# Kernel tuning notes

Measured on AMD Instinct MI355X. Metric: run time of the kernel, lower is better.

## Reference

```python
import jax, jax.numpy as jnp
import numpy as np
from math import factorial

N_SCALES = 4
N_ORI = 4
NA = 9            # spatial_corr_width
H_IMG = 1024
P_REAL = max(2 * N_ORI, 5)


def _polar_grid(H, W):
    ctr_y = int(np.ceil((H + 0.5) / 2)); ctr_x = int(np.ceil((W + 0.5) / 2))
    y = (np.arange(1, H + 1) - ctr_y) / (H / 2.0)
    x = (np.arange(1, W + 1) - ctr_x) / (W / 2.0)
    xr, yr = np.meshgrid(x, y)
    angle = np.arctan2(yr, xr)
    rad = np.sqrt(xr ** 2 + yr ** 2)
    rad[ctr_y - 1, ctr_x - 1] = rad[ctr_y - 1, ctr_x - 2]  # avoid log2(0)
    return np.log2(rad), angle


def _hi(log_rad, shift):
    # raised-cosine sqrt highpass mask: transition over log_rad in [shift-1, shift]
    return np.cos(np.pi / 2.0 * np.clip(log_rad - shift, -1.0, 0.0))


def _lo(log_rad, shift):
    h = _hi(log_rad, shift)
    return np.sqrt(np.clip(1.0 - h * h, 0.0, 1.0))


def _crop(dims):
    # pyrtools-style frequency-domain downsample-by-2 crop indices
    dims = np.asarray(dims)
    ctr = np.ceil((dims + 0.5) / 2).astype(int)
    lodims = np.ceil((dims - 0.5) / 2).astype(int)
    loctr = np.ceil((lodims + 0.5) / 2).astype(int)
    s = ctr - loctr
    return s[0], s[0] + lodims[0], s[1], s[1] + lodims[1]


def _build_pyramid(im):
    """Complex steerable pyramid (frequency-domain), non tight-frame."""
    order = N_ORI - 1
    const = (2.0 ** (2 * order)) * factorial(order) ** 2 / (N_ORI * factorial(2 * order))
    lr, ang = _polar_grid(*im.shape)
    imdft = jnp.fft.fftshift(jnp.fft.fft2(im))
    hipass = jnp.fft.ifft2(jnp.fft.ifftshift(imdft * jnp.asarray(_hi(lr, 0.0), jnp.float32))).real
    lodft = imdft * jnp.asarray(_lo(lr, 0.0), jnp.float32)
    bands, recon_dfts = [], []
    for s in range(N_SCALES):
        recon_dfts.append(lodft)  # spectrum of scales >= s content (partial recon)
        shift = -(s + 1)
        hm = _hi(lr, shift)
        sb = []
        for b in range(N_ORI):
            a = np.mod(ang - np.pi * b / N_ORI + np.pi, 2 * np.pi) - np.pi
            am = 2.0 * np.sqrt(const) * (np.cos(a) ** order) * (np.abs(a) < np.pi / 2)
            banddft = ((-1j) ** order) * lodft * jnp.asarray(hm * am, jnp.float32)
            sb.append(jnp.fft.ifft2(jnp.fft.ifftshift(banddft)))
        bands.append(sb)
        y0, y1, x0, x1 = _crop(lodft.shape)
        lr, ang = lr[y0:y1, x0:x1], ang[y0:y1, x0:x1]
        lodft = lodft[y0:y1, x0:x1] * jnp.asarray(_lo(lr, shift), jnp.float32)
    lowpass = jnp.fft.ifft2(jnp.fft.ifftshift(lodft)).real
    recons = [jnp.fft.ifft2(jnp.fft.ifftshift(d)).real for d in recon_dfts] + [lowpass]
    return hipass, bands, lowpass, recons


def _autocorr(x):
    # central NA x NA window of the autocorrelation, via FFT
    x = x - x.mean()
    H, W = x.shape
    F = jnp.fft.fft2(x)
    p = F.real ** 2 + F.imag ** 2
    ac = jnp.fft.fftshift(jnp.fft.ifft2(p).real) / (H * W)
    lz = NA // 2
    return jax.lax.dynamic_slice(ac, (H // 2 - lz, W // 2 - lz), (NA, NA))


def _skew_kurt(x):
    mu = x.mean()
    c = x - mu
    v = (c * c).mean()
    return (c ** 3).mean() / v ** 1.5, (c ** 4).mean() / v ** 2, v


def _norm_cc(A, B):
    # true cross-correlation of centered columns
    C = A.T @ B / A.shape[0]
    sa = jnp.sqrt((A * A).mean(0)); sb = jnp.sqrt((B * B).mean(0))
    return C / (sa[:, None] * sb[None, :] + 1e-12)


def _expand2(x):
    H, W = x.shape
    F = jnp.fft.fftshift(jnp.fft.fft2(x))
    pad = jnp.zeros((2 * H, 2 * W), F.dtype).at[H // 2:H // 2 + H, W // 2:W // 2 + W].set(F)
    return jnp.fft.ifft2(jnp.fft.ifftshift(pad)) * 4.0


def _ps_stats(image):
    im = image[0, 0]
    hipass, bands, lowpass, recons = _build_pyramid(im)
    sk, ku, var = _skew_kurt(im)
    pix = jnp.stack([im.mean(), var, sk, ku, im.min(), im.max()])
    mags = [[jnp.abs(bands[s][b]) for b in range(N_ORI)] for s in range(N_SCALES)]
    mag_means = jnp.stack([jnp.abs(hipass).mean()]
                          + [mags[s][b].mean() for s in range(N_SCALES) for b in range(N_ORI)]
                          + [jnp.abs(lowpass).mean()])
    mags = [[m - m.mean() for m in row] for row in mags]
    lz = NA // 2
    acm = jnp.zeros((NA, NA, N_SCALES, N_ORI), jnp.float32)
    for s in range(N_SCALES):
        for b in range(N_ORI):
            ac = _autocorr(mags[s][b])
            acm = acm.at[:, :, s, b].set(ac / (ac[lz, lz] + 1e-12))
    acr = jnp.zeros((NA, NA, N_SCALES + 1), jnp.float32)
    skew_r, kurt_r, std_r = [], [], []
    for s, r in enumerate(recons):
        ac = _autocorr(r)
        acr = acr.at[:, :, s].set(ac / (ac[lz, lz] + 1e-12))
        sk_, ku_, v_ = _skew_kurt(r)
        skew_r.append(sk_); kurt_r.append(ku_); std_r.append(jnp.sqrt(v_))
    com = jnp.zeros((N_ORI, N_ORI, N_SCALES + 1), jnp.float32)
    csm = jnp.zeros((N_ORI, N_ORI, N_SCALES), jnp.float32)
    cor = jnp.zeros((P_REAL, P_REAL, N_SCALES + 1), jnp.float32)
    csr = jnp.zeros((2 * N_ORI, P_REAL, N_SCALES), jnp.float32)
    for s in range(N_SCALES):
        M = jnp.stack([m.ravel() for m in mags[s]], 1)                      # (N, Nor) centered magnitudes
        R = jnp.stack([(bands[s][b].real - bands[s][b].real.mean()).ravel()
                       for b in range(N_ORI)], 1)                            # (N, Nor) real parts
        com = com.at[:, :, s].set(_norm_cc(M, M))
        cor = cor.at[:N_ORI, :N_ORI, s].set(_norm_cc(R, R))
        if s < N_SCALES - 1:
            ups = [_expand2(bands[s + 1][b]) for b in range(N_ORI)]
            dp = [u * u / (jnp.abs(u) + 1e-12) for u in ups]                # phase-doubled parents
            Pm = jnp.stack([(jnp.abs(u) - jnp.abs(u).mean()).ravel() for u in ups], 1)
            csm = csm.at[:, :, s].set(_norm_cc(M, Pm))
            RP = jnp.stack([d.real.ravel() for d in dp] + [d.imag.ravel() for d in dp], 1)
            RP = RP - RP.mean(0)
            csr = csr.at[:N_ORI, :2 * N_ORI, s].set(_norm_cc(R, RP))
        else:
            lp = _expand2(lowpass).real
            lp = lp - lp.mean()
            shifts = [lp, jnp.roll(lp, 2, 1), jnp.roll(lp, -2, 1), jnp.roll(lp, 2, 0), jnp.roll(lp, -2, 0)]
            RP = jnp.stack([t.ravel() for t in shifts], 1)                  # 5 shifted lowpass parents
            csr = csr.at[:N_ORI, :5, s].set(_norm_cc(R, RP))
            cor = cor.at[:5, :5, N_SCALES].set(_norm_cc(RP, RP))
    hc = hipass - hipass.mean()
    var_hp = (hc * hc).mean()
    vec = jnp.concatenate([pix, mag_means, acm.ravel(),
                           jnp.stack(skew_r), jnp.stack(kurt_r), acr.ravel(),
                           jnp.stack(std_r), com.ravel(), csm.ravel(),
                           cor.ravel(), csr.ravel(), var_hp[None]])
    return vec[None, None, :].astype(jnp.float32)  # (B=1, C=1, S=2461)


def setup_inputs():
    key = jax.random.key(0)
    return {"image": jax.random.normal(key, (1, 1, H_IMG, H_IMG), jnp.float32)}


def reference(image):
    return _ps_stats(image)
```

## Files before the change

### kernel.cpp

```cpp
#include <hip/hip_runtime.h>
#include <hip/hip_fp16.h>
#include <math.h>

#define PI_F 3.14159265358979323846f

enum { LOP_NONE=0, LOP_R2C, LOP_PAD };
enum { SOP_REAL=0, SOP_HL };

__host__ __device__ constexpr int P4(int a, int b){ return a*4 - a*(a-1)/2 + (b-a); }
__host__ __device__ constexpr int P5(int a, int b){ return a*5 - a*(a-1)/2 + (b-a); }

__device__ __forceinline__ unsigned encf(float f){
  unsigned u = __float_as_uint(f);
  return (u & 0x80000000u) ? ~u : (u | 0x80000000u);
}
__device__ __forceinline__ float decf(unsigned u){
  unsigned b = (u & 0x80000000u) ? (u ^ 0x80000000u) : ~u;
  return __uint_as_float(b);
}
__device__ __forceinline__ float2 cxmul(float2 a, float c, float s){
  return make_float2(c*a.x - s*a.y, c*a.y + s*a.x);
}
__device__ __forceinline__ float2 f2add(float2 a, float2 b){ return make_float2(a.x+b.x, a.y+b.y); }
__device__ __forceinline__ float2 f2sub(float2 a, float2 b){ return make_float2(a.x-b.x, a.y-b.y); }
__device__ __forceinline__ float2 h2f(__half2 h){ return __half22float2(h); }
__device__ __forceinline__ __half2 f2h(float2 f){ return __float22half2_rn(f); }

template<int CNT, int WAVES>
__device__ __forceinline__ void block_reduce_add(float (&acc)[CNT], double* out){
  __shared__ float red[WAVES*CNT];
  int lane = threadIdx.x & 63;
  int wid  = threadIdx.x >> 6;
  #pragma unroll
  for (int k = 0; k < CNT; k++){
    float v = acc[k];
    #pragma unroll
    for (int o = 32; o > 0; o >>= 1) v += __shfl_down(v, o, 64);
    if (lane == 0) red[wid*CNT + k] = v;
  }
  __syncthreads();
  int t = threadIdx.x;
  if (t < CNT){
    double s = 0.0;
    #pragma unroll
    for (int w = 0; w < WAVES; w++) s += (double)red[w*CNT + t];
    atomicAdd(&out[t], s);
  }
  __syncthreads();
}

template<int CNT, int WAVES>
__device__ __forceinline__ void block_reduce_add_sc(float (&acc)[CNT], double* out, float* red){
  __syncthreads();
  int lane = threadIdx.x & 63;
  int wid  = threadIdx.x >> 6;
  #pragma unroll
  for (int k = 0; k < CNT; k++){
    float v = acc[k];
    #pragma unroll
    for (int o = 32; o > 0; o >>= 1) v += __shfl_down(v, o, 64);
    if (lane == 0) red[wid*CNT + k] = v;
  }
  __syncthreads();
  int t = threadIdx.x;
  if (t < CNT){
    double s = 0.0;
    #pragma unroll
    for (int w = 0; w < WAVES; w++) s += (double)red[w*CNT + t];
    atomicAdd(&out[t], s);
  }
}

__device__ __forceinline__ void polar_f(int iy, int ix, float& lr, float& ang){
  float yn = (float)(iy - 512) * (1.f/512.f);
  float xn = (float)(ix - 512) * (1.f/512.f);
  ang = atan2f(yn, xn);
  float rad = (iy == 512 && ix == 512) ? (1.f/512.f) : sqrtf(xn*xn + yn*yn);
  lr = log2f(rad);
}
__device__ __forceinline__ float f_hi(float lr, float shift){
  float v = fminf(fmaxf(lr - shift, -1.f), 0.f);
  return cosf((PI_F*0.5f) * v);
}
__device__ __forceinline__ float f_lo(float lr, float shift){
  float h = f_hi(lr, shift);
  float q = fminf(fmaxf(1.f - h*h, 0.f), 1.f);
  return sqrtf(q);
}
__device__ __forceinline__ float band_am(float ang, int b){
  float a0 = ang - (PI_F*0.25f)*(float)b + PI_F;
  float a = fmodf(a0, 2.f*PI_F);
  if (a < 0.f) a += 2.f*PI_F;
  a -= PI_F;
  float mk = 0.f;
  if (fabsf(a) < PI_F*0.5f){ float c = cosf(a); mk = 1.78885438199983f*c*c*c; }
  return mk;
}

__device__ __forceinline__ void bfly4(float2* v, bool fwd){
  float2 A = f2add(v[0], v[2]), B = f2sub(v[0], v[2]);
  float2 C = f2add(v[1], v[3]), D = f2sub(v[1], v[3]);
  float2 dj = fwd ? make_float2(D.y, -D.x) : make_float2(-D.y, D.x);
  v[0] = f2add(A, C);
  v[1] = f2add(B, dj);
  v[2] = f2sub(A, C);
  v[3] = f2sub(B, dj);
}

template<int N, int T>
__device__ __forceinline__ void fft_rows_body(float2* sm, int t, float dir){
  const bool fwd = (dir < 0.f);
  int Ns = 1;
  if constexpr ((N & 0xAAAAAAAAu) != 0){
    constexpr int NB2 = N/2;
    constexpr int P2 = (NB2 + T - 1)/T;
    float2 a[P2], b[P2];
    #pragma unroll
    for (int p = 0; p < P2; p++){
      int q = t + p*T;
      if (q < NB2){ a[p] = sm[q]; b[p] = sm[q + N/2]; }
    }
    __syncthreads();
    #pragma unroll
    for (int p = 0; p < P2; p++){
      int q = t + p*T;
      if (q < NB2){
        sm[2*q]   = f2add(a[p], b[p]);
        sm[2*q+1] = f2sub(a[p], b[p]);
      }
    }
    __syncthreads();
    Ns = 2;
  }
  constexpr int NB4 = N/4;
  for (; Ns < N; Ns <<= 2){
    float2 v[4];
    int q = t, k = 0;
    if (q < NB4){
      k = q & (Ns - 1);
      #pragma unroll
      for (int r = 0; r < 4; r++) v[r] = sm[q + r*NB4];
      if (k){
        float ang = dir * (PI_F*0.5f) * (float)k / (float)Ns;
        float s1, c1; __sincosf(ang, &s1, &c1);
        float c2 = c1*c1 - s1*s1, s2 = 2.f*c1*s1;
        float c3 = c1*c2 - s1*s2, s3 = c1*s2 + s1*c2;
        v[1] = cxmul(v[1], c1, s1);
        v[2] = cxmul(v[2], c2, s2);
        v[3] = cxmul(v[3], c3, s3);
      }
      bfly4(v, fwd);
    }
    __syncthreads();
    if (q < NB4){
      int dd = ((q - k) << 2) + k;
      sm[dd]        = v[0];
      sm[dd + Ns]   = v[1];
      sm[dd + 2*Ns] = v[2];
      sm[dd + 3*Ns] = v[3];
    }
    __syncthreads();
  }
}

template<int N, int CB, int T>
__device__ __forceinline__ void fft_cols_body(float2* sm, int t, float dir){
  constexpr int LCB = (CB==2)?1:(CB==4)?2:(CB==8)?3:4;
  const bool fwd = (dir < 0.f);
  int Ns = 1;
  if constexpr ((N & 0xAAAAAAAAu) != 0){
    constexpr int NB2 = (N/2)*CB;
    constexpr int P2 = (NB2 + T - 1)/T;
    float2 a[P2], b[P2];
    #pragma unroll
    for (int p = 0; p < P2; p++){
      int q = t + p*T;
      if (q < NB2){
        int c = q & (CB-1), tt = q >> LCB;
        a[p] = sm[tt*CB + c];
        b[p] = sm[(tt + N/2)*CB + c];
      }
    }
    __syncthreads();
    #pragma unroll
    for (int p = 0; p < P2; p++){
      int q = t + p*T;
      if (q < NB2){
        int c = q & (CB-1), tt = q >> LCB;
        sm[(2*tt)*CB + c]   = f2add(a[p], b[p]);
        sm[(2*tt+1)*CB + c] = f2sub(a[p], b[p]);
      }
    }
    __syncthreads();
    Ns = 2;
  }
  constexpr int NB4 = (N/4)*CB;
  constexpr int PB = (NB4 + T - 1)/T;
  for (; Ns < N; Ns <<= 2){
    float2 v[PB][4];
    int kk[PB];
    #pragma unroll
    for (int p = 0; p < PB; p++){
      int q = t + p*T;
      if (q < NB4){
        int c = q & (CB-1), tt = q >> LCB;
        int k = tt & (Ns - 1);
        kk[p] = k;
        #pragma unroll
        for (int r = 0; r < 4; r++) v[p][r] = sm[(tt + r*(N/4))*CB + c];
        if (k){
          float ang = dir * (PI_F*0.5f) * (float)k / (float)Ns;
          float s1, c1; __sincosf(ang, &s1, &c1);
          float c2 = c1*c1 - s1*s1, s2 = 2.f*c1*s1;
          float c3 = c1*c2 - s1*s2, s3 = c1*s2 + s1*c2;
          v[p][1] = cxmul(v[p][1], c1, s1);
          v[p][2] = cxmul(v[p][2], c2, s2);
          v[p][3] = cxmul(v[p][3], c3, s3);
        }
        bfly4(v[p], fwd);
      }
    }
    __syncthreads();
    #pragma unroll
    for (int p = 0; p < PB; p++){
      int q = t + p*T;
      if (q < NB4){
        int c = q & (CB-1), tt = q >> LCB;
        int k = kk[p];
        int dd = ((tt - k) << 2) + k;
        sm[(dd)*CB + c]        = v[p][0];
        sm[(dd + Ns)*CB + c]   = v[p][1];
        sm[(dd + 2*Ns)*CB + c] = v[p][2];
        sm[(dd + 3*Ns)*CB + c] = v[p][3];
      }
    }
    __syncthreads();
  }
}

template<int N>
__global__ __launch_bounds__((N/4 < 64) ? 64 : N/4)
void ps_fft_rows(float2* __restrict__ dst, const void* __restrict__ vsrc,
                 int srcH1, float dir, int xin, int xout, int lop)
{
  constexpr int T = (N/4 < 64) ? 64 : N/4;
  __shared__ float2 sm[N];
  const int t = threadIdx.x;
  const int l = blockIdx.x;
  float2* dline = dst + (size_t)l*N;
  if (lop == LOP_PAD){
    const int q = N/4;
    const int sl = l - q;
    if (sl < 0 || sl >= srcH1){
      for (int j = t; j < N; j += T) dline[j] = make_float2(0.f, 0.f);
      return;
    }
    const float2* s = (const float2*)vsrc + (size_t)sl*srcH1;
    for (int j = t; j < N; j += T){
      int p = j ^ xin;
      sm[j] = (p >= q && p < q + srcH1) ? s[p - q] : make_float2(0.f, 0.f);
    }
  } else if (lop == LOP_R2C){
    const float* s = (const float*)vsrc + (size_t)l*N;
    for (int j = t; j < N; j += T) sm[j] = make_float2(s[j ^ xin], 0.f);
  } else {
    const float2* s = (const float2*)vsrc + (size_t)l*N;
    for (int j = t; j < N; j += T) sm[j] = s[j ^ xin];
  }
  __syncthreads();
  fft_rows_body<N, T>(sm, t, dir);
  for (int j = t; j < N; j += T) dline[j ^ xout] = sm[j];
}

template<int N>
__global__ __launch_bounds__((N/4 < 64) ? 64 : N/4)
void ps_fft_rows_m(__half2* __restrict__ h4, __half2* __restrict__ bandD,
                   const float2* __restrict__ lodS, const float2* __restrict__ lodS1,
                   int nA, int inAHalf, int n, int srcH1,
                   int moffB, float shiftB, int moffC, float shiftC, float scale)
{
  constexpr int T = (N/4 < 64) ? 64 : N/4;
  constexpr int XIN = N/2;
  __shared__ float2 sm[N];
  const int t = threadIdx.x;
  const int l = blockIdx.x & (N-1);
  const int img = blockIdx.x / N;
  __half2* dline;
  if (img < nA)          dline = h4 + (size_t)img*n + (size_t)l*N;
  else if (img < nA + 4) dline = bandD + (size_t)(img - nA)*n + (size_t)l*N;
  else                   dline = h4 + (size_t)(img - 4)*n + (size_t)l*N;

  if (img < nA){
    if (inAHalf){
      const __half2* s = h4 + (size_t)img*n + (size_t)l*N;
      for (int j = t; j < N; j += T) sm[j] = h2f(s[j ^ XIN]);
    } else {
      const float2* s = lodS + (size_t)l*N;
      for (int j = t; j < N; j += T) sm[j] = s[j ^ XIN];
    }
  } else if (img < nA + 4){
    const int b = img - nA;
    const float2* s = lodS + (size_t)l*N;
    for (int j = t; j < N; j += T){
      int x = j ^ XIN;
      float lr, ang; polar_f(moffB + l, moffB + x, lr, ang);
      float mf = f_hi(lr, shiftB) * band_am(ang, b);
      float2 v = s[x];
      sm[j] = make_float2(-mf*v.y, mf*v.x);
    }
  } else {
    const int b = img - nA - 4;
    const int q = N/4;
    const int sl = l - q;
    if (sl < 0 || sl >= srcH1){
      __half2 z = f2h(make_float2(0.f, 0.f));
      for (int j = t; j < N; j += T) dline[j] = z;
      return;
    }
    const float2* s = lodS1 + (size_t)sl*srcH1;
    for (int j = t; j < N; j += T){
      int p = j ^ XIN;
      float2 r = make_float2(0.f, 0.f);
      if (p >= q && p < q + srcH1){
        int x = p - q;
        float lr, ang; polar_f(moffC + sl, moffC + x, lr, ang);
        float mf = f_hi(lr, shiftC) * band_am(ang, b);
        float2 v = s[x];
        r = make_float2(-mf*v.y, mf*v.x);
      }
      sm[j] = r;
    }
  }
  __syncthreads();
  fft_rows_body<N, T>(sm, t, +1.f);
  for (int j = t; j < N; j += T){
    float2 v = sm[j];
    dline[j] = f2h(make_float2(v.x*scale, v.y*scale));
  }
}

template<int N, int CB>
__global__ __launch_bounds__(512)
void ps_fft_cols(float2* __restrict__ dst, const float2* __restrict__ src,
                 __half2* __restrict__ hdst, int hstride,
                 float dir, int xin, int xout, float scale,
                 int sop, float* __restrict__ rdst, double* __restrict__ mout)
{
  constexpr int T = 512;
  constexpr int LCB = (CB==2)?1:(CB==4)?2:(CB==8)?3:4;
  constexpr int NE = N*CB;
  __shared__ float2 sm[NE];
  const int t = threadIdx.x;
  const int c0 = blockIdx.x * CB;
  const float2* sbase = src + c0;

  for (int e = t; e < NE; e += T){
    int j = e >> LCB, c = e & (CB - 1);
    sm[e] = sbase[(size_t)(j ^ xin)*N + c];
  }
  __syncthreads();
  fft_cols_body<N, CB, T>(sm, t, dir);

  if (sop == SOP_HL){
    for (int e = t; e < NE; e += T){
      int j = e >> LCB, c = e & (CB - 1);
      int row = j ^ xout, col = c0 + c;
      float lr, ang; polar_f(row, col, lr, ang);
      float lo = f_lo(lr, 0.f), hi = f_hi(lr, 0.f);
      float2 v = sm[j*CB + c];
      float2 lv = make_float2(v.x*lo, v.y*lo);
      size_t o = (size_t)row*N + col;
      dst[o] = lv;
      hdst[o] = f2h(make_float2(v.x*hi, v.y*hi));
      hdst[(size_t)hstride + o] = f2h(lv);
    }
    return;
  }
  for (int e = t; e < NE; e += T){
    int j = e >> LCB, c = e & (CB - 1);
    rdst[(size_t)(j ^ xout)*N + c0 + c] = sm[j*CB + c].x * scale;
  }
  if (mout){
    float acc[5] = {0.f,0.f,0.f,0.f,0.f};
    for (int e = t; e < NE; e += T){
      float r = sm[e].x * scale, r2 = r*r;
      acc[0] += r; acc[1] += r2; acc[2] += r2*r; acc[3] += r2*r2; acc[4] += fabsf(r);
    }
    block_reduce_add_sc<5, 8>(acc, mout, (float*)sm);
  }
}

template<int N, int CB>
__global__ __launch_bounds__(512)
void ps_fft_cols_m(__half2* __restrict__ h4, __half2* __restrict__ bandD,
                   int nA, int n,
                   float* __restrict__ rdst, int rimg, int rmask,
                   double* __restrict__ mout, int mstride)
{
  constexpr int T = 512;
  constexpr int LCB = (CB==2)?1:(CB==4)?2:(CB==8)?3:4;
  constexpr int NBK = N / CB;
  constexpr int NE = N*CB;
  constexpr int XIN = N/2;
  __shared__ float2 sm[NE];
  const int t = threadIdx.x;
  const int img = blockIdx.x / NBK;
  const int c0 = (blockIdx.x % NBK) * CB;
  __half2* hbase;
  if (img < nA)          hbase = h4 + (size_t)img*n + c0;
  else if (img < nA + 4) hbase = bandD + (size_t)(img - nA)*n + c0;
  else                   hbase = h4 + (size_t)(img - 4)*n + c0;

  for (int e = t; e < NE; e += T){
    int j = e >> LCB, c = e & (CB - 1);
    sm[e] = h2f(hbase[(size_t)(j ^ XIN)*N + c]);
  }
  __syncthreads();
  fft_cols_body<N, CB, T>(sm, t, +1.f);

  if (img < nA){
    if ((rmask >> img) & 1){
      for (int e = t; e < NE; e += T){
        int j = e >> LCB, c = e & (CB - 1);
        rdst[(size_t)img*(size_t)rimg + (size_t)j*N + c0 + c] = sm[j*CB + c].x;
      }
    }
    float acc[5] = {0.f,0.f,0.f,0.f,0.f};
    for (int e = t; e < NE; e += T){
      float r = sm[e].x, r2 = r*r;
      acc[0] += r; acc[1] += r2; acc[2] += r2*r; acc[3] += r2*r2; acc[4] += fabsf(r);
    }
    block_reduce_add_sc<5, 8>(acc, mout + (size_t)img*mstride, (float*)sm);
  } else {
    float mul = (img < nA + 4) ? 1.f : 4.f;
    for (int e = t; e < NE; e += T){
      int j = e >> LCB, c = e & (CB - 1);
      float2 v = sm[j*CB + c];
      hbase[(size_t)j*N + c] = f2h(make_float2(v.x*mul, v.y*mul));
    }
  }
}

#define MAX_AC_TASKS 9
struct AcTaskTab {
  const void* src[MAX_AC_TASKS];
  int isMag[MAX_AC_TASKS];
  int H[MAX_AC_TASKS];
  int npi[MAX_AC_TASKS];
  int nb[MAX_AC_TASKS];
  int stOff[MAX_AC_TASKS];
  int stStride[MAX_AC_TASKS];
  int blkStart[MAX_AC_TASKS+1];
  int nTasks;
};

__global__ __launch_bounds__(256, 1)
void ps_spat_ac_multi(AcTaskTab tt, double* __restrict__ ST)
{
  __shared__ float tile[40*40];
  const int gb = blockIdx.x;
  int tk = 0;
  while (tk + 1 < tt.nTasks && gb >= tt.blkStart[tk+1]) tk++;
  const int lb  = gb - tt.blkStart[tk];
  const int nb  = tt.nb[tk];
  const int img = lb / nb;
  const int b0  = lb - img*nb;
  const int H = tt.H[tk];
  const int n_per_img = tt.npi[tk];
  const int isMag = tt.isMag[tk];
  const void* vsrc = tt.src[tk];
  const int t = threadIdx.x;
  const int tilesX = H >> 5;
  const int tiles = tilesX * tilesX;
  float acc[41];
  #pragma unroll
  for (int k = 0; k < 41; k++) acc[k] = 0.f;

  for (int tl = b0; tl < tiles; tl += nb){
    int by = tl / tilesX, bx = tl - by*tilesX;
    int y0 = by << 5, x0 = bx << 5;
    __syncthreads();
    for (int e = t; e < 40*40; e += 256){
      int ly = e / 40, lx = e - ly*40;
      int gy = (y0 + ly - 4) & (H - 1);
      int gx = (x0 + lx - 4) & (H - 1);
      float v;
      if (isMag){
        float2 c = h2f(((const __half2*)vsrc)[(size_t)img*n_per_img + (size_t)gy*H + gx]);
        v = sqrtf(c.x*c.x + c.y*c.y);
      } else {
        v = ((const float*)vsrc)[(size_t)img*n_per_img + (size_t)gy*H + gx];
      }
      tile[e] = v;
    }
    __syncthreads();
    for (int p = t; p < 32*32; p += 256){
      int py = p >> 5, px = p & 31;
      const float* row0 = tile + (py+4)*40 + (px+4);
      float c = row0[0];
      #pragma unroll
      for (int dx = 0; dx <= 4; dx++)
        acc[dx] += c * row0[dx];
      #pragma unroll
      for (int dy = 1; dy <= 4; dy++){
        const float* rw = row0 + dy*40;
        #pragma unroll
        for (int dx = -4; dx <= 4; dx++)
          acc[5 + (dy-1)*9 + (dx+4)] += c * rw[dx];
      }
    }
  }
  block_reduce_add<41, 4>(acc, ST + tt.stOff[tk] + (size_t)img*tt.stStride[tk]);
}

__global__ __launch_bounds__(256)
void ps_crop_lo(float2* dst, const float2* src, int Hs, int offNew, float shift){
  int Hd = Hs/2;
  int i = blockIdx.x*blockDim.x + threadIdx.x;
  if (i >= Hd*Hd) return;
  int y = i / Hd, x = i - y*Hd;
  float lr, ang; polar_f(offNew + y, offNew + x, lr, ang);
  float mk = f_lo(lr, shift);
  float2 v = src[(y + Hs/4)*Hs + (x + Hs/4)];
  dst[i] = make_float2(v.x*mk, v.y*mk);
}

__global__ void ps_init_mm(unsigned* mm){ mm[0] = 0xFFFFFFFFu; mm[1] = 0u; }

__global__ __launch_bounds__(256, 1)
void ps_im_stats(const float4* __restrict__ x4, int n4, double* out, unsigned* mm){
  float acc[4] = {0.f,0.f,0.f,0.f};
  float mn = INFINITY, mx = -INFINITY;
  for (int i = blockIdx.x*blockDim.x + threadIdx.x; i < n4; i += gridDim.x*blockDim.x){
    float4 v = x4[i];
    float a0 = v.x, a1 = v.y, a2 = v.z, a3 = v.w;
    acc[0] += a0 + a1 + a2 + a3;
    acc[1] += a0*a0 + a1*a1 + a2*a2 + a3*a3;
    acc[2] += a0*a0*a0 + a1*a1*a1 + a2*a2*a2 + a3*a3*a3;
    acc[3] += a0*a0*a0*a0 + a1*a1*a1*a1 + a2*a2*a2*a2 + a3*a3*a3*a3;
    mn = fminf(mn, fminf(fminf(a0,a1), fminf(a2,a3)));
    mx = fmaxf(mx, fmaxf(fmaxf(a0,a1), fmaxf(a2,a3)));
  }
  block_reduce_add<4, 4>(acc, out);
  #pragma unroll
  for (int o = 32; o > 0; o >>= 1){
    mn = fminf(mn, __shfl_down(mn, o, 64));
    mx = fmaxf(mx, __shfl_down(mx, o, 64));
  }
  if ((threadIdx.x & 63) == 0){
    atomicMin(&mm[0], encf(mn));
    atomicMax(&mm[1], encf(mx));
  }
}

struct ScaleATab { const __half2* b[4]; int n[4]; };
__global__ __launch_bounds__(256, 1)
void ps_scaleA_multi(ScaleATab tt, double* __restrict__ ST){
  int s = blockIdx.y;
  int n = tt.n[s];
  if ((size_t)blockIdx.x*blockDim.x >= (size_t)n) return;
  const __half2* bb = tt.b[s];
  double* outp = ST + 64 + s*32;
  float acc[28];
  #pragma unroll
  for (int k = 0; k < 28; k++) acc[k] = 0.f;
  for (int i = blockIdx.x*blockDim.x + threadIdx.x; i < n; i += gridDim.x*blockDim.x){
    float2 v0 = h2f(bb[i]), v1 = h2f(bb[(size_t)n + i]),
           v2 = h2f(bb[2*(size_t)n + i]), v3 = h2f(bb[3*(size_t)n + i]);
    float ab[4] = { sqrtf(v0.x*v0.x+v0.y*v0.y), sqrtf(v1.x*v1.x+v1.y*v1.y),
                    sqrtf(v2.x*v2.x+v2.y*v2.y), sqrtf(v3.x*v3.x+v3.y*v3.y) };
    float re[4] = { v0.x, v1.x, v2.x, v3.x };
    #pragma unroll
    for (int a = 0; a < 4; a++){
      #pragma unroll
      for (int c = a; c < 4; c++){
        acc[P4(a,c)]      += ab[a]*ab[c];
        acc[10 + P4(a,c)] += re[a]*re[c];
      }
      acc[20 + a] += ab[a];
      acc[24 + a] += re[a];
    }
  }
  block_reduce_add<28, 4>(acc, outp);
}
__global__ __launch_bounds__(256, 1)
void ps_scaleB(const __half2* __restrict__ u0, const __half2* __restrict__ u1,
               const __half2* __restrict__ u2, const __half2* __restrict__ u3,
               const __half2* __restrict__ s0, const __half2* __restrict__ s1,
               const __half2* __restrict__ s2, const __half2* __restrict__ s3,
               int n, double* out){
  float acc[72];
  #pragma unroll
  for (int k = 0; k < 72; k++) acc[k] = 0.f;
  for (int i = blockIdx.x*blockDim.x + threadIdx.x; i < n; i += gridDim.x*blockDim.x){
    float2 u[4] = { h2f(u0[i]), h2f(u1[i]), h2f(u2[i]), h2f(u3[i]) };
    float2 bb[4] = { h2f(s0[i]), h2f(s1[i]), h2f(s2[i]), h2f(s3[i]) };
    float au[4], dre[4], dim[4], M[4], R[4];
    #pragma unroll
    for (int c = 0; c < 4; c++){
      float xx = u[c].x, yy = u[c].y;
      float mag = sqrtf(xx*xx + yy*yy);
      float den = mag + 1e-12f;
      au[c] = mag;
      dre[c] = (xx*xx - yy*yy)/den;
      dim[c] = (2.f*xx*yy)/den;
      M[c] = sqrtf(bb[c].x*bb[c].x + bb[c].y*bb[c].y);
      R[c] = bb[c].x;
    }
    #pragma unroll
    for (int c = 0; c < 4; c++){
      acc[c]      += au[c];
      acc[4 + c]  += au[c]*au[c];
      acc[24 + c] += dre[c];
      acc[28 + c] += dim[c];
      acc[32 + c] += dre[c]*dre[c];
      acc[36 + c] += dim[c]*dim[c];
    }
    #pragma unroll
    for (int a = 0; a < 4; a++)
      #pragma unroll
      for (int c = 0; c < 4; c++){
        acc[8 + a*4 + c]  += M[a]*au[c];
        acc[40 + a*4 + c] += R[a]*dre[c];
        acc[56 + a*4 + c] += R[a]*dim[c];
      }
  }
  block_reduce_add<72, 4>(acc, out);
}
__global__ __launch_bounds__(256, 1)
void ps_scaleC(const __half2* __restrict__ s0, const __half2* __restrict__ s1,
               const __half2* __restrict__ s2, const __half2* __restrict__ s3,
               const float* __restrict__ lp, int n, double* out){
  float acc[36];
  #pragma unroll
  for (int k = 0; k < 36; k++) acc[k] = 0.f;
  for (int i = blockIdx.x*blockDim.x + threadIdx.x; i < n; i += gridDim.x*blockDim.x){
    int y = i >> 7, x = i & 127;
    float L[5];
    L[0] = lp[i];
    L[1] = lp[(y << 7) | ((x + 126) & 127)];
    L[2] = lp[(y << 7) | ((x + 2) & 127)];
    L[3] = lp[(((y + 126) & 127) << 7) | x];
    L[4] = lp[(((y + 2) & 127) << 7) | x];
    float R[4] = { h2f(s0[i]).x, h2f(s1[i]).x, h2f(s2[i]).x, h2f(s3[i]).x };
    acc[0] += L[0];
    #pragma unroll
    for (int a = 0; a < 5; a++)
      #pragma unroll
      for (int c = a; c < 5; c++)
        acc[1 + P5(a,c)] += L[a]*L[c];
    #pragma unroll
    for (int a = 0; a < 4; a++)
      #pragma unroll
      for (int j = 0; j < 5; j++)
        acc[16 + a*5 + j] += R[a]*L[j];
  }
  block_reduce_add<36, 4>(acc, out);
}

__device__ __forceinline__ double d_ns(int s){ double h = (double)(1024 >> s); return h*h; }
__device__ __forceinline__ void d_moments(const double* Mo, double n,
                                          double& sk, double& ku, double& var){
  double m = Mo[0]/n, e2 = Mo[1]/n, e3 = Mo[2]/n, e4 = Mo[3]/n;
  var = e2 - m*m;
  double c3 = e3 - 3.0*m*e2 + 2.0*m*m*m;
  double c4 = e4 - 4.0*m*e3 + 6.0*m*m*e2 - 3.0*m*m*m*m;
  sk = c3/pow(var,1.5); ku = c4/(var*var);
}
__device__ __forceinline__ int ac_o(int w){
  int dy = w/9 - 4, dx = w - (w/9)*9 - 4;
  int ady = dy, adx = dx;
  if (dy < 0 || (dy == 0 && dx < 0)){ ady = -dy; adx = -dx; }
  return (ady == 0) ? adx : (5 + (ady-1)*9 + (adx+4));
}

__global__ __launch_bounds__(256)
void ps_finalize(const double* __restrict__ ST, const unsigned* __restrict__ MM,
                 float* __restrict__ out, int out_size){
  int idx = blockIdx.x*blockDim.x + threadIdx.x;
  if (idx >= out_size) return;
  const double n0 = 1048576.0;
  double val = 0.0;

  if (idx <= 5){
    if (idx == 4){ out[4] = decf(MM[0]); return; }
    if (idx == 5){ out[5] = decf(MM[1]); return; }
    double sk, ku, v; d_moments(ST, n0, sk, ku, v);
    val = (idx == 0) ? ST[0]/n0 : (idx == 1) ? v : (idx == 2) ? sk : ku;
  } else if (idx == 6){
    val = ST[8]/n0;
  } else if (idx <= 22){
    int i = idx - 7; int s = i >> 2, b = i & 3;
    val = ST[64 + s*32 + 20 + b] / d_ns(s);
  } else if (idx == 23){
    val = ST[10 + 4*6 + 4] / 4096.0;
  } else if (idx <= 1319){
    int i = idx - 24; int w = i >> 4; int j = i & 15;
    int s = j >> 2, b = j & 3;
    double n = d_ns(s);
    const double* R = ST + 752 + j*48;
    double mu = ST[64 + s*32 + 20 + b]/n, mu2 = mu*mu;
    int o = ac_o(w);
    val = (R[o]/n - mu2) / (R[0]/n - mu2 + 1e-12);
  } else if (idx <= 1329){
    int i = idx - 1320; bool kq = (i >= 5); int r = kq ? i - 5 : i;
    double n = (r == 4) ? 4096.0 : d_ns(r);
    double sk, ku, v; d_moments(ST + 10 + r*6, n, sk, ku, v);
    val = kq ? ku : sk;
  } else if (idx <= 1734){
    int i = idx - 1330; int w = i / 5; int r = i - w*5;
    double n = (r == 4) ? 4096.0 : d_ns(r);
    const double* R = ST + 512 + r*48;
    double mu = ST[10 + r*6]/n, mu2 = mu*mu;
    int o = ac_o(w);
    val = (R[o]/n - mu2) / (R[0]/n - mu2 + 1e-12);
  } else if (idx <= 1739){
    int r = idx - 1735;
    double n = (r == 4) ? 4096.0 : d_ns(r);
    double sk, ku, v; d_moments(ST + 10 + r*6, n, sk, ku, v);
    val = sqrt(v);
  } else if (idx <= 1819){
    int i = idx - 1740; int s = i % 5; int q = i / 5; int a = q >> 2, b = q & 3;
    if (s < 4){
      double n = d_ns(s); const double* A = ST + 64 + s*32;
      double ma = A[20+a]/n, mb = A[20+b]/n;
      double caa = A[P4(a,a)]/n - ma*ma, cbb = A[P4(b,b)]/n - mb*mb;
      int lo = a < b ? a : b, hi = a < b ? b : a;
      double cab = A[P4(lo,hi)]/n - ma*mb;
      val = cab / (sqrt(caa)*sqrt(cbb) + 1e-12);
    }
  } else if (idx <= 1883){
    int i = idx - 1820; int s = i & 3; int q = i >> 2; int a = q >> 2, c = q & 3;
    if (s < 3){
      double n = d_ns(s); const double* A = ST + 64 + s*32; const double* B = ST + 192 + s*80;
      double mM = A[20+a]/n; double sdM = sqrt(A[P4(a,a)]/n - mM*mM);
      double mU = B[c]/n;    double sdU = sqrt(B[4+c]/n - mU*mU);
      val = (B[8 + a*4 + c]/n - mM*mU) / (sdM*sdU + 1e-12);
    }
  } else if (idx <= 2203){
    int i = idx - 1884; int s = i % 5; int q = i / 5; int a = q >> 3, b = q & 7;
    if (s < 4){
      if (a < 4 && b < 4){
        double n = d_ns(s); const double* A = ST + 64 + s*32;
        double ma = A[24+a]/n, mb = A[24+b]/n;
        double caa = A[10+P4(a,a)]/n - ma*ma, cbb = A[10+P4(b,b)]/n - mb*mb;
        int lo = a < b ? a : b, hi = a < b ? b : a;
        double cab = A[10+P4(lo,hi)]/n - ma*mb;
        val = cab / (sqrt(caa)*sqrt(cbb) + 1e-12);
      }
    } else {
      if (a < 5 && b < 5){
        const double* C = ST + 432; const double n3 = 16384.0;
        double lb = C[0]/n3;
        double caa = C[1+P5(a,a)]/n3 - lb*lb, cbb = C[1+P5(b,b)]/n3 - lb*lb;
        int lo = a < b ? a : b, hi = a < b ? b : a;
        double cab = C[1+P5(lo,hi)]/n3 - lb*lb;
        val = cab / (sqrt(caa)*sqrt(cbb) + 1e-12);
      }
    }
  } else if (idx <= 2459){
    int i = idx - 2204; int s = i & 3; int q = i >> 2; int a = q >> 3, c = q & 7;
    if (a < 4){
      double n = d_ns(s); const double* A = ST + 64 + s*32;
      double mR = A[24+a]/n; double sdR = sqrt(A[10+P4(a,a)]/n - mR*mR);
      if (s < 3 && c < 8){
        const double* B = ST + 192 + s*80;
        if (c < 4){
          double md = B[24+c]/n; double sd = sqrt(B[32+c]/n - md*md);
          val = (B[40 + a*4 + c]/n - mR*md) / (sdR*sd + 1e-12);
        } else {
          int cc = c - 4;
          double md = B[28+cc]/n; double sd = sqrt(B[36+cc]/n - md*md);
          val = (B[56 + a*4 + cc]/n - mR*md) / (sdR*sd + 1e-12);
        }
      } else if (s == 3 && c < 5){
        const double* C = ST + 432; const double n3 = 16384.0;
        double lb = C[0]/n3;
        double sdL = sqrt(C[1+P5(c,c)]/n3 - lb*lb);
        val = (C[16 + a*5 + c]/n3 - mR*lb) / (sdR*sdL + 1e-12);
      }
    }
  } else {
    val = ST[5]/n0 - (ST[4]/n0)*(ST[4]/n0);
  }
  out[idx] = (float)val;
}

static void rows_s(int H, float2* dst, const void* src, int srcH1,
                   float dir, int xin, int xout, int lop, hipStream_t st){
  dim3 g(H);
  switch (H){
    case 64:   ps_fft_rows<64>  <<<g, 64,  0, st>>>(dst, src, srcH1, dir, xin, xout, lop); break;
    case 128:  ps_fft_rows<128> <<<g, 64,  0, st>>>(dst, src, srcH1, dir, xin, xout, lop); break;
    case 256:  ps_fft_rows<256> <<<g, 64,  0, st>>>(dst, src, srcH1, dir, xin, xout, lop); break;
    case 512:  ps_fft_rows<512> <<<g, 128, 0, st>>>(dst, src, srcH1, dir, xin, xout, lop); break;
    case 1024: ps_fft_rows<1024><<<g, 256, 0, st>>>(dst, src, srcH1, dir, xin, xout, lop); break;
    default: break;
  }
}
static void cols_s(int H, float2* dst, const float2* src, __half2* hdst, int hstride,
                   float dir, int xin, int xout, float scale,
                   int sop, float* rdst, double* mout, hipStream_t st){
  switch (H){
    case 64:   ps_fft_cols<64,16>  <<<dim3(64/16),  512, 0, st>>>(dst, src, hdst, hstride, dir, xin, xout, scale, sop, rdst, mout); break;
    case 128:  ps_fft_cols<128,16> <<<dim3(128/16), 512, 0, st>>>(dst, src, hdst, hstride, dir, xin, xout, scale, sop, rdst, mout); break;
    case 256:  ps_fft_cols<256,16> <<<dim3(256/16), 512, 0, st>>>(dst, src, hdst, hstride, dir, xin, xout, scale, sop, rdst, mout); break;
    case 512:  ps_fft_cols<512,16> <<<dim3(512/16), 512, 0, st>>>(dst, src, hdst, hstride, dir, xin, xout, scale, sop, rdst, mout); break;
    case 1024: ps_fft_cols<1024,8> <<<dim3(1024/8), 512, 0, st>>>(dst, src, hdst, hstride, dir, xin, xout, scale, sop, rdst, mout); break;
    default: break;
  }
}
static void rows_m(int H, __half2* h4, __half2* bandD, const float2* lodS, const float2* lodS1,
                   int nA, int inAHalf, int nimg, int n, int srcH1,
                   int moffB, float shiftB, int moffC, float shiftC, float scale, hipStream_t st){
  dim3 g(nimg * H);
  switch (H){
    case 128:  ps_fft_rows_m<128> <<<g, 64,  0, st>>>(h4, bandD, lodS, lodS1, nA, inAHalf, n, srcH1, moffB, shiftB, moffC, shiftC, scale); break;
    case 256:  ps_fft_rows_m<256> <<<g, 64,  0, st>>>(h4, bandD, lodS, lodS1, nA, inAHalf, n, srcH1, moffB, shiftB, moffC, shiftC, scale); break;
    case 512:  ps_fft_rows_m<512> <<<g, 128, 0, st>>>(h4, bandD, lodS, lodS1, nA, inAHalf, n, srcH1, moffB, shiftB, moffC, shiftC, scale); break;
    case 1024: ps_fft_rows_m<1024><<<g, 256, 0, st>>>(h4, bandD, lodS, lodS1, nA, inAHalf, n, srcH1, moffB, shiftB, moffC, shiftC, scale); break;
    default: break;
  }
}
static void cols_m(int H, __half2* h4, __half2* bandD, int nA, int nimg, int n,
                   float* rdst, int rimg, int rmask, double* mout, int mstride, hipStream_t st){
  switch (H){
    case 128:  ps_fft_cols_m<128,16> <<<dim3(nimg*(128/16)), 512, 0, st>>>(h4, bandD, nA, n, rdst, rimg, rmask, mout, mstride); break;
    case 256:  ps_fft_cols_m<256,16> <<<dim3(nimg*(256/16)), 512, 0, st>>>(h4, bandD, nA, n, rdst, rimg, rmask, mout, mstride); break;
    case 512:  ps_fft_cols_m<512,16> <<<dim3(nimg*(512/16)), 512, 0, st>>>(h4, bandD, nA, n, rdst, rimg, rmask, mout, mstride); break;
    case 1024: ps_fft_cols_m<1024,8> <<<dim3(nimg*(1024/8)), 512, 0, st>>>(h4, bandD, nA, n, rdst, rimg, rmask, mout, mstride); break;
    default: break;
  }
}

static inline dim3 gr(int n){ return dim3((n + 255)/256); }
static inline int  rblocks(int n){ int b = (n + 255)/256; return b > 512 ? 512 : b; }

#define FWD (-1.0f)
#define INV (+1.0f)

extern "C" void kernel_launch(void* const* d_in, const int* in_sizes, int n_in,
                              void* d_out, int out_size, void* d_ws, size_t ws_size,
                              hipStream_t stream){
  (void)in_sizes; (void)n_in;
  const float* im = (const float*)d_in[0];
  float* out = (float*)d_out;

  const int Hs[5]   = {1024, 512, 256, 128, 64};
  const int offs[5] = {0, 256, 384, 448, 480};

  char* base = (char*)d_ws;
  size_t off = 0;
  auto carve = [&](size_t bytes)->void*{
    void* r = base + off;
    off = (off + bytes + 255) & ~(size_t)255;
    return r;
  };
  const int n0 = 1024*1024;
  float2* lod[5];
  for (int s = 0; s < 5; s++) lod[s] = (float2*)carve((size_t)Hs[s]*Hs[s]*sizeof(float2));
  __half2* band[4];
  for (int s = 0; s < 4; s++) band[s] = (__half2*)carve((size_t)4*Hs[s]*Hs[s]*sizeof(__half2));
  float* reals0 = (float*)carve((size_t)2*n0*sizeof(float));
  float* recon[5];
  recon[0] = reals0 + n0;
  for (int s = 1; s < 5; s++) recon[s] = (float*)carve((size_t)Hs[s]*Hs[s]*sizeof(float));
  float* lp = (float*)carve(128*128*sizeof(float));
  float2* scrF = (float2*)carve((size_t)n0*sizeof(float2));
  __half2* h4 = (__half2*)carve((size_t)6*n0*sizeof(__half2));
  double* ST = (double*)carve(2048*sizeof(double));
  unsigned* MM = (unsigned*)carve(64*sizeof(unsigned));
  if (off > ws_size) return;

  hipMemsetAsync(ST, 0, 2048*sizeof(double), stream);
  ps_init_mm<<<1, 1, 0, stream>>>(MM);
  ps_im_stats<<<256, 256, 0, stream>>>((const float4*)im, n0/4, ST + 0, MM);

  rows_s(1024, scrF, im, 0, FWD, 0, 512, LOP_R2C, stream);
  cols_s(1024, lod[0], scrF, h4, n0, FWD, 0, 512, 1.0f, SOP_HL, nullptr, nullptr, stream);

  for (int s = 0; s < 4; s++){
    int H = Hs[s], n = H*H;
    float invn = 1.0f/((float)H*(float)H);
    ps_crop_lo<<<gr((H/2)*(H/2)), 256, 0, stream>>>(lod[s+1], lod[s], H, offs[s+1], -(float)(s+1));
    int nA = (s == 0) ? 2 : 1;
    int nimg = nA + 4 + ((s < 3) ? 4 : 0);
    rows_m(H, h4, band[s], lod[s], lod[s+1], nA, (s == 0) ? 1 : 0, nimg, n, Hs[s+1],
           offs[s], -(float)(s+1), offs[s+1], -(float)(s+2), invn, stream);
    float* rT = (s == 0) ? reals0 : recon[s];
    int rimg = (s == 0) ? n0 : 0;
    int rmask = (s == 0) ? 2 : 1;
    double* mT = (s == 0) ? (ST + 4) : (ST + 10 + s*6);
    int mstr = (s == 0) ? 6 : 0;
    cols_m(H, h4, band[s], nA, nimg, n, rT, rimg, rmask, mT, mstr, stream);
    if (s < 3){
      __half2* u = h4 + (size_t)nA*n;
      ps_scaleB<<<rblocks(n), 256, 0, stream>>>(u, u+n, u+2*(size_t)n, u+3*(size_t)n,
                                                band[s], band[s]+n, band[s]+2*(size_t)n, band[s]+3*(size_t)n,
                                                n, ST + 192 + s*80);
    }
  }
  rows_s(64, scrF, lod[4], 0, INV, 32, 0, LOP_NONE, stream);
  cols_s(64, nullptr, scrF, nullptr, 0, INV, 32, 0, 1.0f/4096.f, SOP_REAL, recon[4], ST + 34, stream);
  rows_s(128, scrF, lod[4], 64, INV, 64, 0, LOP_PAD, stream);
  cols_s(128, nullptr, scrF, nullptr, 0, INV, 64, 0, 1.0f/4096.f, SOP_REAL, lp, nullptr, stream);
  ps_scaleC<<<rblocks(16384), 256, 0, stream>>>(band[3], band[3]+16384, band[3]+2*16384, band[3]+3*16384,
                                                lp, 16384, ST + 432);

  {
    AcTaskTab tt{};
    int nt = 0, blk = 0;
    auto addTask = [&](const void* src, int isMag, int H, int nimgs, int stOff){
      int tiles = (H>>5)*(H>>5);
      int nb = tiles < 128 ? tiles : 128;
      tt.src[nt] = src; tt.isMag[nt] = isMag; tt.H[nt] = H; tt.npi[nt] = H*H;
      tt.nb[nt] = nb; tt.stOff[nt] = stOff; tt.stStride[nt] = 48;
      tt.blkStart[nt] = blk; blk += nb*nimgs; nt++;
    };
    addTask(band[0], 1, 1024, 4, 752 + 0*4*48);
    addTask(recon[0], 0, 1024, 1, 512 + 0*48);
    addTask(band[1], 1, 512, 4, 752 + 1*4*48);
    addTask(recon[1], 0, 512, 1, 512 + 1*48);
    addTask(band[2], 1, 256, 4, 752 + 2*4*48);
    addTask(recon[2], 0, 256, 1, 512 + 2*48);
    addTask(band[3], 1, 128, 4, 752 + 3*4*48);
    addTask(recon[3], 0, 128, 1, 512 + 3*48);
    addTask(recon[4], 0, 64, 1, 512 + 4*48);
    tt.blkStart[nt] = blk; tt.nTasks = nt;
    ps_spat_ac_multi<<<dim3(blk), 256, 0, stream>>>(tt, ST);
  }

  {
    ScaleATab ta{};
    for (int s = 0; s < 4; s++){ ta.b[s] = band[s]; ta.n[s] = Hs[s]*Hs[s]; }
    ps_scaleA_multi<<<dim3(512, 4), 256, 0, stream>>>(ta, ST);
  }

  ps_finalize<<<gr(out_size), 256, 0, stream>>>(ST, MM, out, out_size);
}
```

Baseline: 391.8 us.

## Share row loads and polar masks across four orientation bands per block

The row-FFT kernel now handles all four orientation bands in one block per row. It loads the source spectrum row and computes the polar and highpass mask once, then loops over the bands applying only the angular mask and running the FFT for each. This removes redundant global loads and transcendental mask evaluations, and cuts the grid size. Separately, the 1024 column kernel now processes two column chunks per block and accumulates the moment statistics across both, halving the number of block reductions and atomics. The cost is fewer, longer blocks, which reduces parallelism, and extra register pressure from the per-thread arrays.

```diff
diff --git a/kernel.cpp b/kernel.cpp
--- a/kernel.cpp
+++ b/kernel.cpp
@@ -281,16 +281,14 @@
 {
   constexpr int T = (N/4 < 64) ? 64 : N/4;
   constexpr int XIN = N/2;
+  constexpr int NP = N / T;
   __shared__ float2 sm[N];
   const int t = threadIdx.x;
   const int l = blockIdx.x & (N-1);
   const int img = blockIdx.x / N;
-  __half2* dline;
-  if (img < nA)          dline = h4 + (size_t)img*n + (size_t)l*N;
-  else if (img < nA + 4) dline = bandD + (size_t)(img - nA)*n + (size_t)l*N;
-  else                   dline = h4 + (size_t)(img - 4)*n + (size_t)l*N;
 
   if (img < nA){
+    __half2* dline = h4 + (size_t)img*n + (size_t)l*N;
     if (inAHalf){
       const __half2* s = h4 + (size_t)img*n + (size_t)l*N;
       for (int j = t; j < N; j += T) sm[j] = h2f(s[j ^ XIN]);
@@ -298,44 +296,94 @@
       const float2* s = lodS + (size_t)l*N;
       for (int j = t; j < N; j += T) sm[j] = s[j ^ XIN];
     }
-  } else if (img < nA + 4){
-    const int b = img - nA;
-    const float2* s = lodS + (size_t)l*N;
+    __syncthreads();
+    fft_rows_body<N, T>(sm, t, +1.f);
     for (int j = t; j < N; j += T){
+      float2 v = sm[j];
+      dline[j] = f2h(make_float2(v.x*scale, v.y*scale));
+    }
+    return;
+  }
+  if (img == nA){
+    float2 rv[NP]; float mfh[NP], angv[NP];
+    #pragma unroll
+    for (int p = 0; p < NP; p++){
+      int j = t + p*T;
       int x = j ^ XIN;
+      rv[p] = lodS[(size_t)l*N + x];
       float lr, ang; polar_f(moffB + l, moffB + x, lr, ang);
-      float mf = f_hi(lr, shiftB) * band_am(ang, b);
-      float2 v = s[x];
-      sm[j] = make_float2(-mf*v.y, mf*v.x);
-    }
-  } else {
-    const int b = img - nA - 4;
+      mfh[p] = f_hi(lr, shiftB);
+      angv[p] = ang;
+    }
+    for (int b = 0; b < 4; b++){
+      #pragma unroll
+      for (int p = 0; p < NP; p++){
+        int j = t + p*T;
+        float mf = mfh[p] * band_am(angv[p], b);
+        sm[j] = make_float2(-mf*rv[p].y, mf*rv[p].x);
+      }
+      __syncthreads();
+      fft_rows_body<N, T>(sm, t, +1.f);
+      __half2* dl = bandD + (size_t)b*n + (size_t)l*N;
+      #pragma unroll
+      for (int p = 0; p < NP; p++){
+        int j = t + p*T;
+        float2 v = sm[j];
+        dl[j] = f2h(make_float2(v.x*scale, v.y*scale));
+      }
+      __syncthreads();
+    }
+    return;
+  }
+  {
     const int q = N/4;
     const int sl = l - q;
     if (sl < 0 || sl >= srcH1){
       __half2 z = f2h(make_float2(0.f, 0.f));
-      for (int j = t; j < N; j += T) dline[j] = z;
+      for (int b = 0; b < 4; b++){
+        __half2* dl = h4 + (size_t)(nA + b)*n + (size_t)l*N;
+        for (int j = t; j < N; j += T) dl[j] = z;
+      }
       return;
     }
-    const float2* s = lodS1 + (size_t)sl*srcH1;
-    for (int j = t; j < N; j += T){
-      int p = j ^ XIN;
-      float2 r = make_float2(0.f, 0.f);
-      if (p >= q && p < q + srcH1){
-        int x = p - q;
+    float2 rv[NP]; float mfh[NP], angv[NP]; bool inr[NP];
+    #pragma unroll
+    for (int p = 0; p < NP; p++){
+      int j = t + p*T;
+      int px = j ^ XIN;
+      bool in = (px >= q && px < q + srcH1);
+      inr[p] = in;
+      mfh[p] = 0.f; angv[p] = 0.f; rv[p] = make_float2(0.f, 0.f);
+      if (in){
+        int x = px - q;
+        rv[p] = lodS1[(size_t)sl*srcH1 + x];
         float lr, ang; polar_f(moffC + sl, moffC + x, lr, ang);
-        float mf = f_hi(lr, shiftC) * band_am(ang, b);
-        float2 v = s[x];
-        r = make_float2(-mf*v.y, mf*v.x);
-      }
-      sm[j] = r;
-    }
-  }
-  __syncthreads();
-  fft_rows_body<N, T>(sm, t, +1.f);
-  for (int j = t; j < N; j += T){
-    float2 v = sm[j];
-    dline[j] = f2h(make_float2(v.x*scale, v.y*scale));
+        mfh[p] = f_hi(lr, shiftC);
+        angv[p] = ang;
+      }
+    }
+    for (int b = 0; b < 4; b++){
+      #pragma unroll
+      for (int p = 0; p < NP; p++){
+        int j = t + p*T;
+        float2 r = make_float2(0.f, 0.f);
+        if (inr[p]){
+          float mf = mfh[p] * band_am(angv[p], b);
+          r = make_float2(-mf*rv[p].y, mf*rv[p].x);
+        }
+        sm[j] = r;
+      }
+      __syncthreads();
+      fft_rows_body<N, T>(sm, t, +1.f);
+      __half2* dl = h4 + (size_t)(nA + b)*n + (size_t)l*N;
+      #pragma unroll
+      for (int p = 0; p < NP; p++){
+        int j = t + p*T;
+        float2 v = sm[j];
+        dl[j] = f2h(make_float2(v.x*scale, v.y*scale));
+      }
+      __syncthreads();
+    }
   }
 }
 
@@ -390,7 +438,7 @@
   }
 }
 
-template<int N, int CB>
+template<int N, int CB, int NCH>
 __global__ __launch_bounds__(512)
 void ps_fft_cols_m(__half2* __restrict__ h4, __half2* __restrict__ bandD,
                    int nA, int n,
@@ -399,46 +447,52 @@
 {
   constexpr int T = 512;
   constexpr int LCB = (CB==2)?1:(CB==4)?2:(CB==8)?3:4;
-  constexpr int NBK = N / CB;
+  constexpr int NBB = N / (CB*NCH);
   constexpr int NE = N*CB;
   constexpr int XIN = N/2;
   __shared__ float2 sm[NE];
   const int t = threadIdx.x;
-  const int img = blockIdx.x / NBK;
-  const int c0 = (blockIdx.x % NBK) * CB;
-  __half2* hbase;
-  if (img < nA)          hbase = h4 + (size_t)img*n + c0;
-  else if (img < nA + 4) hbase = bandD + (size_t)(img - nA)*n + c0;
-  else                   hbase = h4 + (size_t)(img - 4)*n + c0;
-
-  for (int e = t; e < NE; e += T){
-    int j = e >> LCB, c = e & (CB - 1);
-    sm[e] = h2f(hbase[(size_t)(j ^ XIN)*N + c]);
-  }
-  __syncthreads();
-  fft_cols_body<N, CB, T>(sm, t, +1.f);
-
-  if (img < nA){
-    if ((rmask >> img) & 1){
+  const int img = blockIdx.x / NBB;
+  const int cg  = blockIdx.x % NBB;
+  __half2* hb0;
+  if (img < nA)          hb0 = h4 + (size_t)img*n;
+  else if (img < nA + 4) hb0 = bandD + (size_t)(img - nA)*n;
+  else                   hb0 = h4 + (size_t)(img - 4)*n;
+  const bool isA = (img < nA);
+  float acc[5] = {0.f,0.f,0.f,0.f,0.f};
+
+  for (int ch = 0; ch < NCH; ch++){
+    const int c0 = (cg*NCH + ch)*CB;
+    __half2* hbase = hb0 + c0;
+    if (ch) __syncthreads();
+    for (int e = t; e < NE; e += T){
+      int j = e >> LCB, c = e & (CB - 1);
+      sm[e] = h2f(hbase[(size_t)(j ^ XIN)*N + c]);
+    }
+    __syncthreads();
+    fft_cols_body<N, CB, T>(sm, t, +1.f);
+
+    if (isA){
+      if ((rmask >> img) & 1){
+        for (int e = t; e < NE; e += T){
+          int j = e >> LCB, c = e & (CB - 1);
+          rdst[(size_t)img*(size_t)rimg + (size_t)j*N + c0 + c] = sm[j*CB + c].x;
+        }
+      }
+      for (int e = t; e < NE; e += T){
+        float r = sm[e].x, r2 = r*r;
+        acc[0] += r; acc[1] += r2; acc[2] += r2*r; acc[3] += r2*r2; acc[4] += fabsf(r);
+      }
+    } else {
+      float mul = (img < nA + 4) ? 1.f : 4.f;
       for (int e = t; e < NE; e += T){
         int j = e >> LCB, c = e & (CB - 1);
-        rdst[(size_t)img*(size_t)rimg + (size_t)j*N + c0 + c] = sm[j*CB + c].x;
-      }
-    }
-    float acc[5] = {0.f,0.f,0.f,0.f,0.f};
-    for (int e = t; e < NE; e += T){
-      float r = sm[e].x, r2 = r*r;
-      acc[0] += r; acc[1] += r2; acc[2] += r2*r; acc[3] += r2*r2; acc[4] += fabsf(r);
-    }
-    block_reduce_add_sc<5, 8>(acc, mout + (size_t)img*mstride, (float*)sm);
-  } else {
-    float mul = (img < nA + 4) ? 1.f : 4.f;
-    for (int e = t; e < NE; e += T){
-      int j = e >> LCB, c = e & (CB - 1);
-      float2 v = sm[j*CB + c];
-      hbase[(size_t)j*N + c] = f2h(make_float2(v.x*mul, v.y*mul));
-    }
-  }
+        float2 v = sm[j*CB + c];
+        hbase[(size_t)j*N + c] = f2h(make_float2(v.x*mul, v.y*mul));
+      }
+    }
+  }
+  if (isA) block_reduce_add_sc<5, 8>(acc, mout + (size_t)img*mstride, (float*)sm);
 }
 
 #define MAX_AC_TASKS 9
@@ -811,9 +865,9 @@
   }
 }
 static void rows_m(int H, __half2* h4, __half2* bandD, const float2* lodS, const float2* lodS1,
-                   int nA, int inAHalf, int nimg, int n, int srcH1,
+                   int nA, int inAHalf, int nslots, int n, int srcH1,
                    int moffB, float shiftB, int moffC, float shiftC, float scale, hipStream_t st){
-  dim3 g(nimg * H);
+  dim3 g(nslots * H);
   switch (H){
     case 128:  ps_fft_rows_m<128> <<<g, 64,  0, st>>>(h4, bandD, lodS, lodS1, nA, inAHalf, n, srcH1, moffB, shiftB, moffC, shiftC, scale); break;
     case 256:  ps_fft_rows_m<256> <<<g, 64,  0, st>>>(h4, bandD, lodS, lodS1, nA, inAHalf, n, srcH1, moffB, shiftB, moffC, shiftC, scale); break;
@@ -825,10 +879,10 @@
 static void cols_m(int H, __half2* h4, __half2* bandD, int nA, int nimg, int n,
                    float* rdst, int rimg, int rmask, double* mout, int mstride, hipStream_t st){
   switch (H){
-    case 128:  ps_fft_cols_m<128,16> <<<dim3(nimg*(128/16)), 512, 0, st>>>(h4, bandD, nA, n, rdst, rimg, rmask, mout, mstride); break;
-    case 256:  ps_fft_cols_m<256,16> <<<dim3(nimg*(256/16)), 512, 0, st>>>(h4, bandD, nA, n, rdst, rimg, rmask, mout, mstride); break;
-    case 512:  ps_fft_cols_m<512,16> <<<dim3(nimg*(512/16)), 512, 0, st>>>(h4, bandD, nA, n, rdst, rimg, rmask, mout, mstride); break;
-    case 1024: ps_fft_cols_m<1024,8> <<<dim3(nimg*(1024/8)), 512, 0, st>>>(h4, bandD, nA, n, rdst, rimg, rmask, mout, mstride); break;
+    case 128:  ps_fft_cols_m<128,16,1> <<<dim3(nimg*(128/16)),    512, 0, st>>>(h4, bandD, nA, n, rdst, rimg, rmask, mout, mstride); break;
+    case 256:  ps_fft_cols_m<256,16,1> <<<dim3(nimg*(256/16)),    512, 0, st>>>(h4, bandD, nA, n, rdst, rimg, rmask, mout, mstride); break;
+    case 512:  ps_fft_cols_m<512,16,1> <<<dim3(nimg*(512/16)),    512, 0, st>>>(h4, bandD, nA, n, rdst, rimg, rmask, mout, mstride); break;
+    case 1024: ps_fft_cols_m<1024,8,2> <<<dim3(nimg*(1024/16)),   512, 0, st>>>(h4, bandD, nA, n, rdst, rimg, rmask, mout, mstride); break;
     default: break;
   }
 }
@@ -884,8 +938,9 @@
     float invn = 1.0f/((float)H*(float)H);
     ps_crop_lo<<<gr((H/2)*(H/2)), 256, 0, stream>>>(lod[s+1], lod[s], H, offs[s+1], -(float)(s+1));
     int nA = (s == 0) ? 2 : 1;
-    int nimg = nA + 4 + ((s < 3) ? 4 : 0);
-    rows_m(H, h4, band[s], lod[s], lod[s+1], nA, (s == 0) ? 1 : 0, nimg, n, Hs[s+1],
+    int nslots = nA + 1 + ((s < 3) ? 1 : 0);
+    int nimg   = nA + 4 + ((s < 3) ? 4 : 0);
+    rows_m(H, h4, band[s], lod[s], lod[s+1], nA, (s == 0) ? 1 : 0, nslots, n, Hs[s+1],
            offs[s], -(float)(s+1), offs[s+1], -(float)(s+2), invn, stream);
     float* rT = (s == 0) ? reals0 : recon[s];
     int rimg = (s == 0) ? n0 : 0;
```

Result: slower. 411.4 us (+5.0%).
